# Performance work log

Measured on AMD Instinct MI355X. Metric: run time of the kernel, lower is better.

The kernel has to match this reference:

```python
import jax, jax.numpy as jnp
import numpy as np
from jax import lax

B, F_A, F_S, H, T = 4096, 64, 256, 1024, 64
DT = 0.05


def setup_inputs() -> dict:
    key = jax.random.key(0)
    k1, k2, k3, k4, k5, k6 = jax.random.split(key, 6)
    scale1 = 1.0 / np.sqrt(F_A + F_S)
    scale2 = 1.0 / np.sqrt(H)
    return {
        "ts": jnp.arange(T, dtype=jnp.float32) * DT,
        "actions": jax.random.normal(k1, (B, F_A, T), dtype=jnp.float32),
        "y0": jax.random.normal(k2, (B, F_S), dtype=jnp.float32),
        "W1": jax.random.normal(k3, (F_A + F_S, H), dtype=jnp.float32) * scale1,
        "b1": jnp.zeros((H,), dtype=jnp.float32),
        "W2": jax.random.normal(k4, (H, F_S), dtype=jnp.float32) * scale2,
        "b2": jnp.zeros((F_S,), dtype=jnp.float32),
        "dt": jnp.float32(DT),
    }


def reference(ts, actions, y0, W1, b1, W2, b2, dt):
    # ODEFunc: f(cat([a, y], -1)) with 2-layer tanh MLP; Euler: y' = y + dt*f
    def f(a, y):
        s = jnp.concatenate([a, y], axis=-1)        # (B, F_a+F_s)
        h = jnp.tanh(s @ W1 + b1)                   # (B, H)
        return h @ W2 + b2                          # (B, F_s)

    acts_t = jnp.transpose(actions, (2, 0, 1))      # (T, B, F_a)

    def step(y, a):
        y_next = y + dt * f(a, y)
        return y_next, y_next

    # y(ts[0]) = y0; T-1 euler steps driven by actions at times 0..T-2
    _, ys = lax.scan(step, y0, acts_t[:-1])         # (T-1, B, F_s)
    traj = jnp.concatenate([y0[None], ys], axis=0)  # (T, B, F_s)
    return jnp.transpose(traj, (1, 2, 0))           # (B, F_s, T)
```

## Files before the change

### kernel.cpp

```cpp
#include <hip/hip_runtime.h>

typedef _Float16 v8h __attribute__((ext_vector_type(8)));
typedef float v4f __attribute__((ext_vector_type(4)));

#define NT 512
#define XSTR 344
#define HSTR 1032

static constexpr size_t ATT_BYTES_NEEDED = 2359296ull + 4096ull * 64 * 64 * 4;

#define MFMA16 __builtin_amdgcn_mfma_f32_16x16x32_f16

#define GLOAD(dst, base, vo) \
  asm volatile("global_load_dwordx4 %0, %1, %2" : "=v"(dst) : "v"(vo), "s"(base))
#define VMW_(n) asm volatile("s_waitcnt vmcnt(" #n ")" ::: "memory")
#define VMW(n) do { VMW_(n); __builtin_amdgcn_sched_barrier(0); } while (0)
#define LGKMBAR() do { asm volatile("s_waitcnt lgkmcnt(0)" ::: "memory"); \
  __builtin_amdgcn_s_barrier(); } while (0)

__device__ __forceinline__ float tanh_fast(float a) {
  float e = __expf(2.0f * a);
  return 1.0f - __fdividef(2.0f, e + 1.0f);
}

extern "C" __global__ void conv_w(const float* __restrict__ W1,
                                  const float* __restrict__ W2,
                                  _Float16* __restrict__ ws) {
  int i = blockIdx.x * 256 + threadIdx.x;
  if (i < 327680) {
    int j = i & 7, lane = (i >> 3) & 63, w = (i >> 9) & 7, gp = i >> 12;
    int g = lane >> 4, l15 = lane & 15;
    int ph = gp / 10, p = gp % 10;
    float v = W1[(p * 32 + g * 8 + j) * 1024 + ph * 128 + w * 16 + l15];
    _Float16 hh = (_Float16)v;
    ws[i] = hh;
    ws[327680 + i] = (_Float16)((v - (float)hh) * 2048.f);
  } else {
    int iq = i - 655360;
    if (iq >= 0) {
      int j = iq & 7, t = (iq >> 3) & 511, s = iq >> 12;
      int lane = t & 63, wave = t >> 6, g = lane >> 4, l15 = lane & 15;
      int p = s >> 1, ph2 = s & 1;
      float v = W2[(p * 32 + g * 8 + j) * 256 + ph2 * 128 + wave * 16 + l15];
      _Float16 hh = (_Float16)v;
      ws[655360 + iq] = hh;
      ws[917504 + iq] = (_Float16)((v - (float)hh) * 2048.f);
    }
  }
}

extern "C" __global__ void conv_a(const float* __restrict__ actions,
                                  float* __restrict__ att) {
  size_t o = (size_t)blockIdx.x * 256 + threadIdx.x;
  int f = (int)(o & 63);
  int b = (int)((o >> 6) & 4095);
  int t = (int)(o >> 18);
  att[o] = actions[((size_t)b * 64 + f) * 64 + t];
}

#define G1BODY(p, RF, N, RD0) do { \
    VMW(N); \
    v8h bh = B1H[(p) % 5], bl = B1L[(p) % 5]; \
    if (RF) { GLOAD(B1H[(p) % 5], w1hB, vo1); GLOAD(B1L[(p) % 5], w1lB, vo1); \
              vo1 += 8192; if (vo1 == vend1) vo1 = tid16; } \
    v8h xch = Xh[(p) & 1], xcl = Xl[(p) & 1]; \
    if ((p) < 9) { \
      Xh[((p) + 1) & 1] = *(const v8h*)&xHs[xbase + ((p) + 1) * 32]; \
      Xl[((p) + 1) & 1] = *(const v8h*)&xLs[xbase + ((p) + 1) * 32]; \
    } else if (RD0) { \
      Xh[0] = *(const v8h*)&xHs[xbase]; \
      Xl[0] = *(const v8h*)&xLs[xbase]; \
    } \
    accH = MFMA16(xch, bh, accH, 0, 0, 0); \
    accM = MFMA16(xch, bl, accM, 0, 0, 0); \
    accM = MFMA16(xcl, bh, accM, 0, 0, 0); \
  } while (0)

#define B2PRO(k, off) do { \
    GLOAD(B2H0[k], w2hB, (off)); \
    GLOAD(B2L0[k], w2lB, (off)); \
    GLOAD(B2H1[k], w2hB, (off) + 8192); \
    GLOAD(B2L1[k], w2lB, (off) + 8192); \
  } while (0)

#define G2BODY(j, s3, par, RF, RD, N) do { \
    VMW(N); \
    v8h bh0 = B2H0[s3], bl0 = B2L0[s3]; \
    v8h bh1 = B2H1[s3], bl1 = B2L1[s3]; \
    if (RF) { \
      GLOAD(B2H0[s3], w2hB, vo2); GLOAD(B2L0[s3], w2lB, vo2); \
      GLOAD(B2H1[s3], w2hB, vo2 + 8192); GLOAD(B2L1[s3], w2lB, vo2 + 8192); \
      vo2 += 16384; if (vo2 == vend2) vo2 = tid16; \
    } \
    v8h hch = Hh[par], hcl = Hl_[par]; \
    if (RD) { \
      Hh[(par) ^ 1]  = *(const v8h*)&hHs[hbase + hnx]; \
      Hl_[(par) ^ 1] = *(const v8h*)&hLs[hbase + hnx]; \
      hnx = (hnx + 32) & 1023; \
    } \
    c0H = MFMA16(hch, bh0, c0H, 0, 0, 0); \
    c0M = MFMA16(hch, bl0, c0M, 0, 0, 0); \
    c0M = MFMA16(hcl, bh0, c0M, 0, 0, 0); \
    c1H = MFMA16(hch, bh1, c1H, 0, 0, 0); \
    c1M = MFMA16(hch, bl1, c1M, 0, 0, 0); \
    c1M = MFMA16(hcl, bh1, c1M, 0, 0, 0); \
  } while (0)

extern "C" __global__ void __launch_bounds__(NT, 2)
ode_kernel(const float* __restrict__ actions, const float* __restrict__ att,
           const float* __restrict__ y0,
           const float* __restrict__ b1f, const float* __restrict__ b2f,
           const float* __restrict__ dtp, const _Float16* __restrict__ ws,
           float* __restrict__ out)
{
  __shared__ __align__(16) _Float16 xHs[16 * XSTR], xLs[16 * XSTR];
  __shared__ __align__(16) _Float16 hHs[16 * HSTR], hLs[16 * HSTR];
  __shared__ float b1s[1024];

  const int tid  = threadIdx.x;
  const int lane = tid & 63;
  const int l15  = lane & 15, g = lane >> 4;
  const int nloc = (tid >> 6) * 16 + l15;
  const int b0   = blockIdx.x * 16;
  const float dt = dtp[0];
  const int tid16 = tid * 16;

  const int rot8  = (blockIdx.x >> 3) & 7;
  const int rot2c = (blockIdx.x >> 3) & 31;
  const int vend1 = tid16 + 655360;
  const int vend2 = tid16 + 524288;

  const _Float16* w1hB = ws;
  const _Float16* w1lB = ws + 327680;
  const _Float16* w2hB = ws + 655360;
  const _Float16* w2lB = ws + 917504;

  for (int i = tid; i < 1024; i += NT) b1s[i] = b1f[i];
  const float b2r0 = b2f[nloc], b2r1 = b2f[128 + nloc];

  float ya[4], yb[4];
  #pragma unroll
  for (int j = 0; j < 4; ++j) {
    int m = g * 4 + j;
    ya[j] = y0[(size_t)(b0 + m) * 256 + nloc];
    yb[j] = y0[(size_t)(b0 + m) * 256 + 128 + nloc];
    out[((size_t)((b0 + m) * 256 + nloc)) * 64] = ya[j];
    out[((size_t)((b0 + m) * 256 + 128 + nloc)) * 64] = yb[j];
  }

  const int xbase = l15 * XSTR + g * 8;
  const int hbase = l15 * HSTR + g * 8;

  v8h B1H[5], B1L[5];
  v8h B2H0[3], B2L0[3], B2H1[3], B2L1[3];
  v8h Xh[2], Xl[2], Hh[2], Hl_[2];

  const int g1p0 = tid16 + rot8 * 81920;

  #pragma unroll
  for (int s = 0; s < 5; ++s) {
    GLOAD(B1H[s], w1hB, g1p0 + s * 8192);
    GLOAD(B1L[s], w1lB, g1p0 + s * 8192);
  }

  #pragma unroll 1
  for (int t = 0; t < 63; ++t) {
    #pragma unroll
    for (int it = 0; it < 2; ++it) {
      int o = tid + NT * it;
      int m = o >> 6, k = o & 63;
      float v = att ? att[((size_t)t * 4096 + b0 + m) * 64 + k]
                    : actions[((size_t)(b0 + m) * 64 + k) * 64 + t];
      _Float16 hh = (_Float16)v;
      xHs[m * XSTR + k] = hh;
      xLs[m * XSTR + k] = (_Float16)((v - (float)hh) * 2048.f);
    }
    #pragma unroll
    for (int j = 0; j < 4; ++j) {
      int m = g * 4 + j;
      _Float16 h0 = (_Float16)ya[j];
      xHs[m * XSTR + 64 + nloc] = h0;
      xLs[m * XSTR + 64 + nloc] = (_Float16)((ya[j] - (float)h0) * 2048.f);
      _Float16 h1 = (_Float16)yb[j];
      xHs[m * XSTR + 192 + nloc] = h1;
      xLs[m * XSTR + 192 + nloc] = (_Float16)((yb[j] - (float)h1) * 2048.f);
    }
    LGKMBAR();

    Xh[0] = *(const v8h*)&xHs[xbase];
    Xl[0] = *(const v8h*)&xLs[xbase];

    int vo1 = g1p0 + 5 * 8192;

    #pragma unroll 1
    for (int ph = 0; ph < 7; ++ph) {
      const int pha = (ph + rot8) & 7;
      const float bb = b1s[pha * 128 + nloc];
      v4f accH = v4f{bb, bb, bb, bb};
      v4f accM = v4f{0.f, 0.f, 0.f, 0.f};
      #pragma unroll
      for (int p = 0; p < 10; ++p) G1BODY(p, 1, 8, 1);
      #pragma unroll
      for (int j = 0; j < 4; ++j) {
        float v = accH[j] + accM[j] * (1.f / 2048.f);
        float th = tanh_fast(v);
        _Float16 hh = (_Float16)th;
        int m = g * 4 + j;
        hHs[m * HSTR + pha * 128 + nloc] = hh;
        hLs[m * HSTR + pha * 128 + nloc] = (_Float16)((th - (float)hh) * 2048.f);
      }
    }
    {
      const int pha = (7 + rot8) & 7;
      const float bb = b1s[pha * 128 + nloc];
      v4f accH = v4f{bb, bb, bb, bb};
      v4f accM = v4f{0.f, 0.f, 0.f, 0.f};
      #pragma unroll
      for (int p = 0; p < 6; ++p) G1BODY(p, (p) < 5, 8, 1);
      G1BODY(6, 0, 6, 1);
      B2PRO(0, tid16 + ((rot2c + 0) & 31) * 16384);
      G1BODY(7, 0, 8, 1);
      B2PRO(1, tid16 + ((rot2c + 1) & 31) * 16384);
      G1BODY(8, 0, 10, 1);
      B2PRO(2, tid16 + ((rot2c + 2) & 31) * 16384);
      G1BODY(9, 0, 12, 0);
      #pragma unroll
      for (int j = 0; j < 4; ++j) {
        float v = accH[j] + accM[j] * (1.f / 2048.f);
        float th = tanh_fast(v);
        _Float16 hh = (_Float16)th;
        int m = g * 4 + j;
        hHs[m * HSTR + pha * 128 + nloc] = hh;
        hLs[m * HSTR + pha * 128 + nloc] = (_Float16)((th - (float)hh) * 2048.f);
      }
    }
    LGKMBAR();

    int hnx = ((rot2c + 1) & 31) * 32;
    Hh[0]  = *(const v8h*)&hHs[hbase + rot2c * 32];
    Hl_[0] = *(const v8h*)&hLs[hbase + rot2c * 32];

    int vo2 = tid16 + ((rot2c + 3) & 31) * 16384;

    v4f c0H = v4f{b2r0, b2r0, b2r0, b2r0}, c0M = v4f{0.f, 0.f, 0.f, 0.f};
    v4f c1H = v4f{b2r1, b2r1, b2r1, b2r1}, c1M = v4f{0.f, 0.f, 0.f, 0.f};

    #pragma unroll 1
    for (int jj = 0; jj < 4; ++jj) {
      const int jb = jj * 6;
      G2BODY(jb + 0, 0, 0, 1, 1, 8);
      G2BODY(jb + 1, 1, 1, 1, 1, 8);
      G2BODY(jb + 2, 2, 0, 1, 1, 8);
      G2BODY(jb + 3, 0, 1, 1, 1, 8);
      G2BODY(jb + 4, 1, 0, 1, 1, 8);
      G2BODY(jb + 5, 2, 1, 1, 1, 8);
    }
    G2BODY(24, 0, 0, 1, 1, 8);
    G2BODY(25, 1, 1, 1, 1, 8);
    G2BODY(26, 2, 0, 1, 1, 8);
    G2BODY(27, 0, 1, 1, 1, 8);
    G2BODY(28, 1, 0, 1, 1, 8);
    G2BODY(29, 2, 1, 0, 1, 8);
    G2BODY(30, 0, 0, 0, 1, 4);
    G2BODY(31, 1, 1, 0, 0, 0);

    #pragma unroll
    for (int j = 0; j < 4; ++j) {
      int m = g * 4 + j;
      float yn0 = ya[j] + dt * (c0H[j] + c0M[j] * (1.f / 2048.f));
      ya[j] = yn0;
      out[((size_t)((b0 + m) * 256 + nloc)) * 64 + (t + 1)] = yn0;
      float yn1 = yb[j] + dt * (c1H[j] + c1M[j] * (1.f / 2048.f));
      yb[j] = yn1;
      out[((size_t)((b0 + m) * 256 + 128 + nloc)) * 64 + (t + 1)] = yn1;
    }
    if (t < 62) {
      #pragma unroll
      for (int s = 0; s < 5; ++s) {
        GLOAD(B1H[s], w1hB, g1p0 + s * 8192);
        GLOAD(B1L[s], w1lB, g1p0 + s * 8192);
      }
    }
  }
}

extern "C" void kernel_launch(void* const* d_in, const int* in_sizes, int n_in,
                              void* d_out, int out_size, void* d_ws, size_t ws_size,
                              hipStream_t stream) {
  const float* actions = (const float*)d_in[1];
  const float* y0      = (const float*)d_in[2];
  const float* W1      = (const float*)d_in[3];
  const float* b1      = (const float*)d_in[4];
  const float* W2      = (const float*)d_in[5];
  const float* b2      = (const float*)d_in[6];
  const float* dtp     = (const float*)d_in[7];
  float* out = (float*)d_out;
  _Float16* ws = (_Float16*)d_ws;

  const bool use_att = ws_size >= ATT_BYTES_NEEDED;
  float* att = use_att ? (float*)((char*)d_ws + 2359296) : nullptr;

  hipLaunchKernelGGL(conv_w, dim3(3584), dim3(256), 0, stream, W1, W2, ws);
  if (use_att)
    hipLaunchKernelGGL(conv_a, dim3(65536), dim3(256), 0, stream, actions, att);
  hipLaunchKernelGGL(ode_kernel, dim3(256), dim3(NT), 0, stream,
                     actions, att, y0, b1, b2, dtp, ws, out);
}
```

Before: 2.266 ms.

## Split batch into 8-row blocks with 512 workgroups and transposed output pass

```diff
diff --git a/kernel.cpp b/kernel.cpp
--- a/kernel.cpp
+++ b/kernel.cpp
@@ -7,7 +7,9 @@
 #define XSTR 344
 #define HSTR 1032
 
-static constexpr size_t ATT_BYTES_NEEDED = 2359296ull + 4096ull * 64 * 64 * 4;
+static constexpr size_t ATT_BYTES_NEEDED = 2359296ull + 67108864ull;
+static constexpr size_t YSC_OFF = 69468160ull;
+static constexpr size_t YSC_BYTES_NEEDED = YSC_OFF + 268435456ull;
 
 #define MFMA16 __builtin_amdgcn_mfma_f32_16x16x32_f16
 
@@ -58,6 +60,22 @@
   att[o] = actions[((size_t)b * 64 + f) * 64 + t];
 }
 
+extern "C" __global__ void tr_out(const float* __restrict__ ysc,
+                                  float* __restrict__ out) {
+  __shared__ float tile[256][65];
+  const int b = blockIdx.x, tid = threadIdx.x;
+  #pragma unroll 8
+  for (int t = 0; t < 64; ++t)
+    tile[tid][t] = ysc[(size_t)t * 1048576 + (size_t)b * 256 + tid];
+  __syncthreads();
+  const int w = tid >> 6, l = tid & 63;
+  #pragma unroll 8
+  for (int cc = 0; cc < 64; ++cc) {
+    int c = w * 64 + cc;
+    out[(size_t)b * 16384 + (size_t)c * 64 + l] = tile[c][l];
+  }
+}
+
 #define G1BODY(p, RF, N, RD0) do { \
     VMW(N); \
     v8h bh = B1H[(p) % 5], bl = B1L[(p) % 5]; \
@@ -106,12 +124,196 @@
     c1M = MFMA16(hcl, bh1, c1M, 0, 0, 0); \
   } while (0)
 
+#define XWRITE(m, va, vb) do { \
+    _Float16 h0 = (_Float16)(va); \
+    xHs[(m) * XSTR + 64 + nloc] = h0; \
+    xLs[(m) * XSTR + 64 + nloc] = (_Float16)(((va) - (float)h0) * 2048.f); \
+    _Float16 h1 = (_Float16)(vb); \
+    xHs[(m) * XSTR + 192 + nloc] = h1; \
+    xLs[(m) * XSTR + 192 + nloc] = (_Float16)(((vb) - (float)h1) * 2048.f); \
+  } while (0)
+
 extern "C" __global__ void __launch_bounds__(NT, 2)
-ode_kernel(const float* __restrict__ actions, const float* __restrict__ att,
-           const float* __restrict__ y0,
-           const float* __restrict__ b1f, const float* __restrict__ b2f,
-           const float* __restrict__ dtp, const _Float16* __restrict__ ws,
-           float* __restrict__ out)
+ode8(const float* __restrict__ att, const float* __restrict__ y0,
+     const float* __restrict__ b1f, const float* __restrict__ b2f,
+     const float* __restrict__ dtp, const _Float16* __restrict__ ws,
+     float* __restrict__ ysc)
+{
+  __shared__ __align__(16) _Float16 xHs[8 * XSTR], xLs[8 * XSTR];
+  __shared__ __align__(16) _Float16 hHs[8 * HSTR], hLs[8 * HSTR];
+  __shared__ float b1s[1024];
+
+  const int tid  = threadIdx.x;
+  const int lane = tid & 63;
+  const int l15  = lane & 15, g = lane >> 4;
+  const int act  = g < 2;
+  const int nloc = (tid >> 6) * 16 + l15;
+  const int b0   = blockIdx.x * 8;
+  const float dt = dtp[0];
+  const int tid16 = tid * 16;
+
+  const int rot8  = (blockIdx.x >> 3) & 7;
+  const int rot2c = (blockIdx.x >> 3) & 31;
+  const int vend1 = tid16 + 655360;
+  const int vend2 = tid16 + 524288;
+
+  const _Float16* w1hB = ws;
+  const _Float16* w1lB = ws + 327680;
+  const _Float16* w2hB = ws + 655360;
+  const _Float16* w2lB = ws + 917504;
+
+  for (int i = tid; i < 1024; i += NT) b1s[i] = b1f[i];
+  const float b2r0 = b2f[nloc], b2r1 = b2f[128 + nloc];
+
+  float ya[4], yb[4];
+  #pragma unroll
+  for (int j = 0; j < 4; ++j) {
+    int m = (g * 4 + j) & 7;
+    ya[j] = y0[(size_t)(b0 + m) * 256 + nloc];
+    yb[j] = y0[(size_t)(b0 + m) * 256 + 128 + nloc];
+    if (act) {
+      ysc[(size_t)(b0 + m) * 256 + nloc] = ya[j];
+      ysc[(size_t)(b0 + m) * 256 + 128 + nloc] = yb[j];
+    }
+  }
+
+  const int xbase = l15 * XSTR + g * 8;
+  const int hbase = l15 * HSTR + g * 8;
+
+  v8h B1H[5], B1L[5];
+  v8h B2H0[3], B2L0[3], B2H1[3], B2L1[3];
+  v8h Xh[2], Xl[2], Hh[2], Hl_[2];
+
+  const int g1p0 = tid16 + rot8 * 81920;
+  #pragma unroll
+  for (int s = 0; s < 5; ++s) {
+    GLOAD(B1H[s], w1hB, g1p0 + s * 8192);
+    GLOAD(B1L[s], w1lB, g1p0 + s * 8192);
+  }
+
+  #pragma unroll 1
+  for (int t = 0; t < 63; ++t) {
+    {
+      int m = tid >> 6, k = tid & 63;
+      float v = att[((size_t)t * 4096 + b0 + m) * 64 + k];
+      _Float16 hh = (_Float16)v;
+      xHs[m * XSTR + k] = hh;
+      xLs[m * XSTR + k] = (_Float16)((v - (float)hh) * 2048.f);
+    }
+    if (act) {
+      #pragma unroll
+      for (int j = 0; j < 4; ++j) XWRITE(g * 4 + j, ya[j], yb[j]);
+    }
+    LGKMBAR();
+
+    Xh[0] = *(const v8h*)&xHs[xbase];
+    Xl[0] = *(const v8h*)&xLs[xbase];
+
+    int vo1 = g1p0 + 5 * 8192;
+
+    #pragma unroll 1
+    for (int ph = 0; ph < 7; ++ph) {
+      const int pha = (ph + rot8) & 7;
+      const float bb = b1s[pha * 128 + nloc];
+      v4f accH = v4f{bb, bb, bb, bb};
+      v4f accM = v4f{0.f, 0.f, 0.f, 0.f};
+      #pragma unroll
+      for (int p = 0; p < 10; ++p) G1BODY(p, 1, 8, 1);
+      if (act) {
+        #pragma unroll
+        for (int j = 0; j < 4; ++j) {
+          float v = accH[j] + accM[j] * (1.f / 2048.f);
+          float th = tanh_fast(v);
+          _Float16 hh = (_Float16)th;
+          int m = g * 4 + j;
+          hHs[m * HSTR + pha * 128 + nloc] = hh;
+          hLs[m * HSTR + pha * 128 + nloc] = (_Float16)((th - (float)hh) * 2048.f);
+        }
+      }
+    }
+    {
+      const int pha = (7 + rot8) & 7;
+      const float bb = b1s[pha * 128 + nloc];
+      v4f accH = v4f{bb, bb, bb, bb};
+      v4f accM = v4f{0.f, 0.f, 0.f, 0.f};
+      #pragma unroll
+      for (int p = 0; p < 6; ++p) G1BODY(p, (p) < 5, 8, 1);
+      G1BODY(6, 0, 6, 1);
+      B2PRO(0, tid16 + ((rot2c + 0) & 31) * 16384);
+      G1BODY(7, 0, 8, 1);
+      B2PRO(1, tid16 + ((rot2c + 1) & 31) * 16384);
+      G1BODY(8, 0, 10, 1);
+      B2PRO(2, tid16 + ((rot2c + 2) & 31) * 16384);
+      G1BODY(9, 0, 12, 0);
+      if (act) {
+        #pragma unroll
+        for (int j = 0; j < 4; ++j) {
+          float v = accH[j] + accM[j] * (1.f / 2048.f);
+          float th = tanh_fast(v);
+          _Float16 hh = (_Float16)th;
+          int m = g * 4 + j;
+          hHs[m * HSTR + pha * 128 + nloc] = hh;
+          hLs[m * HSTR + pha * 128 + nloc] = (_Float16)((th - (float)hh) * 2048.f);
+        }
+      }
+    }
+    LGKMBAR();
+
+    int hnx = ((rot2c + 1) & 31) * 32;
+    Hh[0]  = *(const v8h*)&hHs[hbase + rot2c * 32];
+    Hl_[0] = *(const v8h*)&hLs[hbase + rot2c * 32];
+
+    int vo2 = tid16 + ((rot2c + 3) & 31) * 16384;
+
+    v4f c0H = v4f{b2r0, b2r0, b2r0, b2r0}, c0M = v4f{0.f, 0.f, 0.f, 0.f};
+    v4f c1H = v4f{b2r1, b2r1, b2r1, b2r1}, c1M = v4f{0.f, 0.f, 0.f, 0.f};
+
+    #pragma unroll 1
+    for (int jj = 0; jj < 4; ++jj) {
+      const int jb = jj * 6;
+      G2BODY(jb + 0, 0, 0, 1, 1, 8);
+      G2BODY(jb + 1, 1, 1, 1, 1, 8);
+      G2BODY(jb + 2, 2, 0, 1, 1, 8);
+      G2BODY(jb + 3, 0, 1, 1, 1, 8);
+      G2BODY(jb + 4, 1, 0, 1, 1, 8);
+      G2BODY(jb + 5, 2, 1, 1, 1, 8);
+    }
+    G2BODY(24, 0, 0, 1, 1, 8);
+    G2BODY(25, 1, 1, 1, 1, 8);
+    G2BODY(26, 2, 0, 1, 1, 8);
+    G2BODY(27, 0, 1, 1, 1, 8);
+    G2BODY(28, 1, 0, 1, 1, 8);
+    G2BODY(29, 2, 1, 0, 1, 8);
+    G2BODY(30, 0, 0, 0, 1, 4);
+    G2BODY(31, 1, 1, 0, 0, 0);
+
+    #pragma unroll
+    for (int j = 0; j < 4; ++j) {
+      int m = g * 4 + j;
+      float yn0 = ya[j] + dt * (c0H[j] + c0M[j] * (1.f / 2048.f));
+      float yn1 = yb[j] + dt * (c1H[j] + c1M[j] * (1.f / 2048.f));
+      ya[j] = yn0; yb[j] = yn1;
+      if (act) {
+        ysc[(size_t)(t + 1) * 1048576 + (size_t)(b0 + m) * 256 + nloc] = yn0;
+        ysc[(size_t)(t + 1) * 1048576 + (size_t)(b0 + m) * 256 + 128 + nloc] = yn1;
+      }
+    }
+    if (t < 62) {
+      #pragma unroll
+      for (int s = 0; s < 5; ++s) {
+        GLOAD(B1H[s], w1hB, g1p0 + s * 8192);
+        GLOAD(B1L[s], w1lB, g1p0 + s * 8192);
+      }
+    }
+  }
+}
+
+extern "C" __global__ void __launch_bounds__(NT, 2)
+ode16(const float* __restrict__ actions, const float* __restrict__ att,
+      const float* __restrict__ y0,
+      const float* __restrict__ b1f, const float* __restrict__ b2f,
+      const float* __restrict__ dtp, const _Float16* __restrict__ ws,
+      float* __restrict__ out)
 {
   __shared__ __align__(16) _Float16 xHs[16 * XSTR], xLs[16 * XSTR];
   __shared__ __align__(16) _Float16 hHs[16 * HSTR], hLs[16 * HSTR];
@@ -156,7 +358,6 @@
   v8h Xh[2], Xl[2], Hh[2], Hl_[2];
 
   const int g1p0 = tid16 + rot8 * 81920;
-
   #pragma unroll
   for (int s = 0; s < 5; ++s) {
     GLOAD(B1H[s], w1hB, g1p0 + s * 8192);
@@ -176,15 +377,7 @@
       xLs[m * XSTR + k] = (_Float16)((v - (float)hh) * 2048.f);
     }
     #pragma unroll
-    for (int j = 0; j < 4; ++j) {
-      int m = g * 4 + j;
-      _Float16 h0 = (_Float16)ya[j];
-      xHs[m * XSTR + 64 + nloc] = h0;
-      xLs[m * XSTR + 64 + nloc] = (_Float16)((ya[j] - (float)h0) * 2048.f);
-      _Float16 h1 = (_Float16)yb[j];
-      xHs[m * XSTR + 192 + nloc] = h1;
-      xLs[m * XSTR + 192 + nloc] = (_Float16)((yb[j] - (float)h1) * 2048.f);
-    }
+    for (int j = 0; j < 4; ++j) XWRITE(g * 4 + j, ya[j], yb[j]);
     LGKMBAR();
 
     Xh[0] = *(const v8h*)&xHs[xbase];
@@ -298,11 +491,20 @@
   _Float16* ws = (_Float16*)d_ws;
 
   const bool use_att = ws_size >= ATT_BYTES_NEEDED;
+  const bool use_ysc = ws_size >= YSC_BYTES_NEEDED;
   float* att = use_att ? (float*)((char*)d_ws + 2359296) : nullptr;
+  float* ysc = use_ysc ? (float*)((char*)d_ws + YSC_OFF) : nullptr;
 
   hipLaunchKernelGGL(conv_w, dim3(3584), dim3(256), 0, stream, W1, W2, ws);
   if (use_att)
     hipLaunchKernelGGL(conv_a, dim3(65536), dim3(256), 0, stream, actions, att);
-  hipLaunchKernelGGL(ode_kernel, dim3(256), dim3(NT), 0, stream,
-                     actions, att, y0, b1, b2, dtp, ws, out);
-}
+
+  if (use_att && use_ysc) {
+    hipLaunchKernelGGL(ode8, dim3(512), dim3(NT), 0, stream,
+                       att, y0, b1, b2, dtp, ws, ysc);
+    hipLaunchKernelGGL(tr_out, dim3(4096), dim3(256), 0, stream, ysc, out);
+  } else {
+    hipLaunchKernelGGL(ode16, dim3(256), dim3(NT), 0, stream,
+                       actions, att, y0, b1, b2, dtp, ws, out);
+  }
+}
```

New measurement: 2.869 ms. 26.6% more time.
